# Optimization experiments

Measured on AMD Instinct MI355X. Metric: run time of the kernel, lower is better.

Reference implementation:

```python
import jax, jax.numpy as jnp
import numpy as np

D_MODEL = 1024
NUM_HEADS = 16
HEAD_DIM = D_MODEL // NUM_HEADS
B, L = 2, 2048


def setup_inputs() -> dict:
    key = jax.random.key(0)
    ks = jax.random.split(key, 9)
    s = 0.02
    return {
        "query": jax.random.normal(ks[0], (B, L, D_MODEL), dtype=jnp.float32),
        "key": jax.random.normal(ks[1], (B, L, D_MODEL), dtype=jnp.float32),
        "value": jax.random.normal(ks[2], (B, L, D_MODEL), dtype=jnp.float32),
        "mask": jax.random.randint(ks[3], (B, L), 0, 2, dtype=jnp.int32),
        "Wq": jax.random.normal(ks[4], (D_MODEL, D_MODEL), dtype=jnp.float32) * s,
        "Wk": jax.random.normal(ks[5], (D_MODEL, D_MODEL), dtype=jnp.float32) * s,
        "Wv": jax.random.normal(ks[6], (D_MODEL, D_MODEL), dtype=jnp.float32) * s,
        "Wo": jax.random.normal(ks[7], (D_MODEL, D_MODEL), dtype=jnp.float32) * s,
        "bo": jnp.zeros((D_MODEL,), dtype=jnp.float32),
    }


def _split_heads(x):
    # (B, L, d_model) -> (B, H, L, head_dim)
    b, l, _ = x.shape
    return x.reshape(b, l, NUM_HEADS, HEAD_DIM).transpose(0, 2, 1, 3)


def reference(query, key, value, mask, Wq, Wk, Wv, Wo, bo):
    # nn.Linear(bias=False): x @ W.T
    q = _split_heads(query @ Wq.T)   # (B, H, L, hd)
    k = _split_heads(key @ Wk.T)
    v = _split_heads(value @ Wv.T)

    scores = jnp.einsum("bhqd,bhkd->bhqk", q, k) / jnp.sqrt(jnp.float32(HEAD_DIM))
    # padding mask over keys: (B, L) -> (B, 1, 1, L); 0 = pad -> -inf
    keep = (mask[:, None, None, :] != 0)
    scores = jnp.where(keep, scores, -jnp.inf)

    attn = jax.nn.softmax(scores, axis=-1)
    # original zeroes NaN rows (fully-masked query rows)
    attn = jnp.where(jnp.isnan(attn), jnp.zeros_like(attn), attn)
    # dropout is identity in eval/reference mode

    ctx = jnp.einsum("bhqk,bhkd->bhqd", attn, v)           # (B, H, L, hd)
    ctx = ctx.transpose(0, 2, 1, 3).reshape(B, L, D_MODEL)  # combine heads
    return ctx @ Wo.T + bo
```

## Files before the change

kernel.cpp:

```cpp
#include <hip/hip_runtime.h>

typedef unsigned short u16;
typedef __bf16 bf16x8 __attribute__((ext_vector_type(8)));
typedef __bf16 bf16x4 __attribute__((ext_vector_type(4)));
typedef float floatx4 __attribute__((ext_vector_type(4)));
typedef u16 u16x4 __attribute__((ext_vector_type(4)));

#define MEG ((size_t)(1u << 20))

__device__ __forceinline__ u16 f2bf(float f) {
  unsigned int u = __float_as_uint(f);
  u += 0x7fffu + ((u >> 16) & 1u);
  return (u16)(u >> 16);
}

__device__ __forceinline__ void load_lds16(const u16* g, u16* l) {
  __builtin_amdgcn_global_load_lds((const __attribute__((address_space(1))) unsigned int*)g,
                                   (__attribute__((address_space(3))) unsigned int*)l,
                                   16, 0, 0);
}

__global__ __launch_bounds__(256) void cvt7(
    const float* __restrict__ s0, const float* __restrict__ s1,
    const float* __restrict__ s2, const float* __restrict__ s3,
    const float* __restrict__ s4, const float* __restrict__ s5,
    const float* __restrict__ s6, u16* __restrict__ dst)
{
  size_t e = ((size_t)blockIdx.x * 256 + threadIdx.x) * 4;
  unsigned m = (unsigned)(e >> 20);
  const float* s; size_t off;
  if (m < 4)       { s = s0; off = e; }
  else if (m < 8)  { s = s1; off = e - 4 * MEG; }
  else if (m < 12) { s = s2; off = e - 8 * MEG; }
  else if (m < 13) { s = s3; off = e - 12 * MEG; }
  else if (m < 14) { s = s4; off = e - 13 * MEG; }
  else if (m < 15) { s = s5; off = e - 14 * MEG; }
  else             { s = s6; off = e - 15 * MEG; }
  float4 f = *reinterpret_cast<const float4*>(s + off);
  u16x4 o;
  o.x = f2bf(f.x); o.y = f2bf(f.y); o.z = f2bf(f.z); o.w = f2bf(f.w);
  *reinterpret_cast<u16x4*>(dst + e) = o;
}

template<int IT, bool OUT_BF16, bool ADD_BIAS, bool VT>
__global__ __launch_bounds__(256) void gemm_bt(
    const u16* __restrict__ Abase, const u16* __restrict__ Bbase,
    const float* __restrict__ bias, void* __restrict__ Cbase,
    u16* __restrict__ VtB,
    int M, int N, int K, long zA, long zB, long zC)
{
  __shared__ __align__(16) u16 As[IT * 32 * 64];
  __shared__ __align__(16) u16 Bs[128 * 64];
  const int tid = threadIdx.x;
  const int w = tid >> 6, ln = tid & 63;
  const int lm = ln & 15, lq = ln >> 4;
  const int wm = w >> 1, wn = w & 1;
  const long m0 = (long)blockIdx.y * (IT * 32), n0 = (long)blockIdx.x * 128;
  const u16* A = Abase + (size_t)blockIdx.z * (size_t)zA;
  const u16* B = Bbase + (size_t)blockIdx.z * (size_t)zB;

  const int r0 = tid >> 3;
  const int kc = (tid & 7) ^ (r0 & 7);
  const u16* gA = A + (m0 + r0) * (long)K + kc * 8;
  const u16* gB = B + (n0 + r0) * (long)K + kc * 8;
  const long rstep = 32L * K;

  const int sl0 = (lq ^ (lm & 7)) * 8;
  const int sl1 = ((4 + lq) ^ (lm & 7)) * 8;
  const u16* ab0 = &As[(wm * (IT * 16) + lm) * 64 + sl0];
  const u16* ab1 = &As[(wm * (IT * 16) + lm) * 64 + sl1];
  const u16* bb0 = &Bs[(wn * 64 + lm) * 64 + sl0];
  const u16* bb1 = &Bs[(wn * 64 + lm) * 64 + sl1];

  const floatx4 z4 = {0.f, 0.f, 0.f, 0.f};
  floatx4 acc[IT][4];
#pragma unroll
  for (int i = 0; i < IT; ++i)
#pragma unroll
    for (int j = 0; j < 4; ++j) acc[i][j] = z4;

  for (int k0 = 0; k0 < K; k0 += 64) {
#pragma unroll
    for (int t = 0; t < IT; ++t)
      load_lds16(gA + t * rstep, &As[(t * 256 + w * 64) * 8]);
#pragma unroll
    for (int t = 0; t < 4; ++t)
      load_lds16(gB + t * rstep, &Bs[(t * 256 + w * 64) * 8]);
    gA += 64; gB += 64;
    __syncthreads();
    bf16x8 af[IT][2], bfr[4][2];
#pragma unroll
    for (int i = 0; i < IT; ++i) {
      af[i][0] = *reinterpret_cast<const bf16x8*>(ab0 + i * 1024);
      af[i][1] = *reinterpret_cast<const bf16x8*>(ab1 + i * 1024);
    }
#pragma unroll
    for (int j = 0; j < 4; ++j) {
      bfr[j][0] = *reinterpret_cast<const bf16x8*>(bb0 + j * 1024);
      bfr[j][1] = *reinterpret_cast<const bf16x8*>(bb1 + j * 1024);
    }
#pragma unroll
    for (int i = 0; i < IT; ++i)
#pragma unroll
      for (int j = 0; j < 4; ++j) {
        acc[i][j] = __builtin_amdgcn_mfma_f32_16x16x32_bf16(af[i][0], bfr[j][0], acc[i][j], 0, 0, 0);
        acc[i][j] = __builtin_amdgcn_mfma_f32_16x16x32_bf16(af[i][1], bfr[j][1], acc[i][j], 0, 0, 0);
      }
    __syncthreads();
  }

  if (VT && blockIdx.z == 2) {
#pragma unroll
    for (int i = 0; i < IT; ++i) {
      long row = m0 + wm * (IT * 16) + i * 16 + lq * 4;
      int bq = (int)(row >> 11);
      int l  = (int)(row & 2047);
#pragma unroll
      for (int j = 0; j < 4; ++j) {
        long col = n0 + wn * 64 + j * 16 + lm;
        int hh = (int)(col >> 6), dd = (int)(col & 63);
        u16x4 o;
        o.x = f2bf(acc[i][j][0]); o.y = f2bf(acc[i][j][1]);
        o.z = f2bf(acc[i][j][2]); o.w = f2bf(acc[i][j][3]);
        *reinterpret_cast<u16x4*>(&VtB[((size_t)(bq * 16 + hh)) * 131072 +
                                       (size_t)dd * 2048 + l]) = o;
      }
    }
    return;
  }

#pragma unroll
  for (int i = 0; i < IT; ++i) {
    long row = m0 + wm * (IT * 16) + i * 16 + lq * 4;
#pragma unroll
    for (int j = 0; j < 4; ++j) {
      long col = n0 + wn * 64 + j * 16 + lm;
#pragma unroll
      for (int r = 0; r < 4; ++r) {
        float v = acc[i][j][r];
        if (ADD_BIAS) v += bias[col];
        size_t idx = (size_t)(row + r) * (size_t)N + (size_t)col;
        if (OUT_BF16) (((u16*)Cbase) + (size_t)blockIdx.z * (size_t)zC)[idx] = f2bf(v);
        else ((float*)Cbase)[idx] = v;
      }
    }
  }
}

__global__ __launch_bounds__(256, 4) void attn_kernel(
    const u16* __restrict__ Qp, const u16* __restrict__ Kp,
    const u16* __restrict__ Vt, const int* __restrict__ mask,
    u16* __restrict__ ctx)
{
  __shared__ __align__(16) u16 Ks[64 * 64];
  __shared__ __align__(16) u16 Vts[64 * 64];
  __shared__ __align__(16) u16 Ps[4 * 32 * 64];
  __shared__ __align__(16) u16 mball[2048];

  const int tid = threadIdx.x;
  const int w = tid >> 6, ln = tid & 63;
  const int lm = ln & 15, lq = ln >> 4;
  const int bh = blockIdx.y, b = bh >> 4, h = bh & 15;
  const int q0 = blockIdx.x * 128;

  const u16* Qh = Qp + (size_t)b * 2048 * 1024 + h * 64;
  const u16* Kh = Kp + (size_t)b * 2048 * 1024 + h * 64;
  const u16* Vth = Vt + (size_t)bh * 64 * 2048;

  const int* mrowp = mask + b * 2048;
#pragma unroll
  for (int t = 0; t < 8; ++t) {
    int i = t * 256 + tid;
    mball[i] = (mrowp[i] != 0) ? (u16)0 : (u16)0xFF80;
  }

  bf16x8 qf[2][2];
#pragma unroll
  for (int m = 0; m < 2; ++m) {
    int qrow = q0 + w * 32 + m * 16 + lm;
    qf[m][0] = *reinterpret_cast<const bf16x8*>(Qh + (size_t)qrow * 1024 + lq * 8);
    qf[m][1] = *reinterpret_cast<const bf16x8*>(Qh + (size_t)qrow * 1024 + 32 + lq * 8);
  }

  const int sl0 = (lq ^ (lm & 7)) * 8;
  const int sl1 = ((4 + lq) ^ (lm & 7)) * 8;
  const u16* kb0 = &Ks[lm * 64 + sl0];
  const u16* kb1 = &Ks[lm * 64 + sl1];
  const u16* vb0 = &Vts[lm * 64 + sl0];
  const u16* vb1 = &Vts[lm * 64 + sl1];
  u16* Pw = &Ps[w * 2048];
  u16* pwr[4];
#pragma unroll
  for (int n = 0; n < 4; ++n) pwr[n] = &Pw[lm * 64 + (((4 * n + lq) ^ lm) * 4)];
  const u16* prd[4];
#pragma unroll
  for (int t = 0; t < 4; ++t)
    prd[t] = &Pw[lm * 64 + (((8 * (t >> 1) + 2 * lq + (t & 1)) ^ lm) * 4)];
  const u16* mbi = mball + lq * 4;

  const int r0 = tid >> 3;
  const int kc = (tid & 7) ^ (r0 & 7);
  const u16* gK0 = Kh + (size_t)r0 * 1024 + kc * 8;
  const u16* gK1 = gK0 + 32 * 1024;
  const u16* gV0 = Vth + (size_t)r0 * 2048 + kc * 8;
  const u16* gV1 = gV0 + 32 * 2048;

  const floatx4 z4 = {0.f, 0.f, 0.f, 0.f};
  floatx4 O[2][4];
#pragma unroll
  for (int m = 0; m < 2; ++m)
#pragma unroll
    for (int j = 0; j < 4; ++j) O[m][j] = z4;
  float psum[2] = {0.f, 0.f};
  const float SCL = 0.18033688011112042f;

  for (int it = 0; it < 32; ++it) {
    load_lds16(gK0, &Ks[(w * 64) * 8]);
    load_lds16(gK1, &Ks[(256 + w * 64) * 8]);
    load_lds16(gV0, &Vts[(w * 64) * 8]);
    load_lds16(gV1, &Vts[(256 + w * 64) * 8]);
    gK0 += 64 * 1024; gK1 += 64 * 1024; gV0 += 64; gV1 += 64;
    __syncthreads();

    bf16x8 kf[4][2], vf[4][2];
#pragma unroll
    for (int n = 0; n < 4; ++n) {
      kf[n][0] = *reinterpret_cast<const bf16x8*>(kb0 + n * 1024);
      kf[n][1] = *reinterpret_cast<const bf16x8*>(kb1 + n * 1024);
    }
#pragma unroll
    for (int j = 0; j < 4; ++j) {
      vf[j][0] = *reinterpret_cast<const bf16x8*>(vb0 + j * 1024);
      vf[j][1] = *reinterpret_cast<const bf16x8*>(vb1 + j * 1024);
    }
    float mb4[4][4];
#pragma unroll
    for (int n = 0; n < 4; ++n) {
      u16x4 mv = *reinterpret_cast<const u16x4*>(mbi + n * 16);
      mb4[n][0] = __uint_as_float((unsigned)mv.x << 16);
      mb4[n][1] = __uint_as_float((unsigned)mv.y << 16);
      mb4[n][2] = __uint_as_float((unsigned)mv.z << 16);
      mb4[n][3] = __uint_as_float((unsigned)mv.w << 16);
    }

#pragma unroll
    for (int m = 0; m < 2; ++m) {
      floatx4 S[4];
#pragma unroll
      for (int n = 0; n < 4; ++n) {
        S[n] = __builtin_amdgcn_mfma_f32_16x16x32_bf16(kf[n][0], qf[m][0], z4, 0, 0, 0);
        S[n] = __builtin_amdgcn_mfma_f32_16x16x32_bf16(kf[n][1], qf[m][1], S[n], 0, 0, 0);
      }

#pragma unroll
      for (int n = 0; n < 4; ++n) {
        float p0 = __builtin_amdgcn_exp2f(fmaf(S[n][0], SCL, mb4[n][0]));
        float p1 = __builtin_amdgcn_exp2f(fmaf(S[n][1], SCL, mb4[n][1]));
        float p2 = __builtin_amdgcn_exp2f(fmaf(S[n][2], SCL, mb4[n][2]));
        float p3 = __builtin_amdgcn_exp2f(fmaf(S[n][3], SCL, mb4[n][3]));
        psum[m] += (p0 + p1) + (p2 + p3);
        unsigned u0 = __float_as_uint(p0) + 0x8000u;
        unsigned u1 = __float_as_uint(p1) + 0x8000u;
        unsigned u2 = __float_as_uint(p2) + 0x8000u;
        unsigned u3 = __float_as_uint(p3) + 0x8000u;
        uint2 pk;
        pk.x = __builtin_amdgcn_perm(u1, u0, 0x07060302u);
        pk.y = __builtin_amdgcn_perm(u3, u2, 0x07060302u);
        *reinterpret_cast<uint2*>(pwr[n] + m * 1024) = pk;
      }

#pragma unroll
      for (int h2 = 0; h2 < 2; ++h2) {
        bf16x4 pa = *reinterpret_cast<const bf16x4*>(prd[2 * h2] + m * 1024);
        bf16x4 pb = *reinterpret_cast<const bf16x4*>(prd[2 * h2 + 1] + m * 1024);
        bf16x8 pf = __builtin_shufflevector(pa, pb, 0, 1, 2, 3, 4, 5, 6, 7);
#pragma unroll
        for (int j = 0; j < 4; ++j)
          O[m][j] = __builtin_amdgcn_mfma_f32_16x16x32_bf16(pf, vf[j][h2], O[m][j], 0, 0, 0);
      }
    }
    mbi += 64;
    __syncthreads();
  }

#pragma unroll
  for (int m = 0; m < 2; ++m) {
    float s = psum[m];
    s += __shfl_xor(s, 16, 64);
    s += __shfl_xor(s, 32, 64);
#pragma unroll
    for (int r = 0; r < 4; ++r) {
      int srcl = (ln & 48) | (lq * 4 + r);
      float inv = 1.0f / __shfl(s, srcl, 64);
      int row = q0 + w * 32 + m * 16 + lq * 4 + r;
      size_t base = ((size_t)b * 2048 + row) * 1024 + h * 64 + lm;
#pragma unroll
      for (int j = 0; j < 4; ++j)
        ctx[base + j * 16] = f2bf(O[m][j][r] * inv);
    }
  }
}

extern "C" void kernel_launch(void* const* d_in, const int* in_sizes, int n_in,
                              void* d_out, int out_size, void* d_ws, size_t ws_size,
                              hipStream_t stream) {
  const float* q  = (const float*)d_in[0];
  const float* k  = (const float*)d_in[1];
  const float* v  = (const float*)d_in[2];
  const int*   mk = (const int*)  d_in[3];
  const float* wq = (const float*)d_in[4];
  const float* wk = (const float*)d_in[5];
  const float* wv = (const float*)d_in[6];
  const float* wo = (const float*)d_in[7];
  const float* bo = (const float*)d_in[8];

  u16* ws16 = (u16*)d_ws;
  u16* Xq  = ws16;
  u16* Wq  = ws16 + 12 * MEG;
  u16* Wo  = ws16 + 15 * MEG;
  u16* Qp  = ws16 + 16 * MEG;
  u16* Kp  = ws16 + 20 * MEG;
  u16* Vt  = ws16 + 24 * MEG;
  u16* ctx = ws16 + 4 * MEG;

  cvt7<<<dim3(16384), dim3(256), 0, stream>>>(q, k, v, wq, wk, wv, wo, ws16);

  gemm_bt<4, true, false, true><<<dim3(8, 32, 3), dim3(256), 0, stream>>>(
      Xq, Wq, nullptr, (void*)Qp, Vt, 4096, 1024, 1024,
      (long)(4 * MEG), (long)MEG, (long)(4 * MEG));

  attn_kernel<<<dim3(16, 32), dim3(256), 0, stream>>>(Qp, Kp, Vt, mk, ctx);

  gemm_bt<2, false, true, false><<<dim3(8, 64, 1), dim3(256), 0, stream>>>(
      ctx, Wo, bo, d_out, nullptr, 4096, 1024, 1024, 0, 0, 0);
}
```

Measured before the change: 230.8 us.

## Use single-wave attention blocks loading K/V fragments directly from global memory

Shrinks the attention kernel from four-wave blocks with shared K/V tiles in LDS to one-wave blocks. Each wave now loads its K and V MFMA fragments straight from global memory, which removes the LDS staging and both block barriers per iteration. The trade-off is that every wave re-reads K/V instead of four waves sharing them, giving roughly four times the K/V global/L2 traffic. It also guards the final normalization against a zero row sum, so fully masked rows produce zero.

```diff
diff --git a/kernel.cpp b/kernel.cpp
--- a/kernel.cpp
+++ b/kernel.cpp
@@ -147,21 +147,18 @@
   }
 }
 
-__global__ __launch_bounds__(256, 4) void attn_kernel(
+__global__ __launch_bounds__(64) void attn_kernel(
     const u16* __restrict__ Qp, const u16* __restrict__ Kp,
     const u16* __restrict__ Vt, const int* __restrict__ mask,
     u16* __restrict__ ctx)
 {
-  __shared__ __align__(16) u16 Ks[64 * 64];
-  __shared__ __align__(16) u16 Vts[64 * 64];
-  __shared__ __align__(16) u16 Ps[4 * 32 * 64];
+  __shared__ __align__(16) u16 Ps[32 * 64];
   __shared__ __align__(16) u16 mball[2048];
 
-  const int tid = threadIdx.x;
-  const int w = tid >> 6, ln = tid & 63;
+  const int ln = threadIdx.x;
   const int lm = ln & 15, lq = ln >> 4;
   const int bh = blockIdx.y, b = bh >> 4, h = bh & 15;
-  const int q0 = blockIdx.x * 128;
+  const int q0 = blockIdx.x * 32;
 
   const u16* Qh = Qp + (size_t)b * 2048 * 1024 + h * 64;
   const u16* Kh = Kp + (size_t)b * 2048 * 1024 + h * 64;
@@ -169,41 +166,36 @@
 
   const int* mrowp = mask + b * 2048;
 #pragma unroll
-  for (int t = 0; t < 8; ++t) {
-    int i = t * 256 + tid;
+  for (int t = 0; t < 32; ++t) {
+    int i = t * 64 + ln;
     mball[i] = (mrowp[i] != 0) ? (u16)0 : (u16)0xFF80;
   }
 
   bf16x8 qf[2][2];
 #pragma unroll
   for (int m = 0; m < 2; ++m) {
-    int qrow = q0 + w * 32 + m * 16 + lm;
+    int qrow = q0 + m * 16 + lm;
     qf[m][0] = *reinterpret_cast<const bf16x8*>(Qh + (size_t)qrow * 1024 + lq * 8);
     qf[m][1] = *reinterpret_cast<const bf16x8*>(Qh + (size_t)qrow * 1024 + 32 + lq * 8);
   }
 
-  const int sl0 = (lq ^ (lm & 7)) * 8;
-  const int sl1 = ((4 + lq) ^ (lm & 7)) * 8;
-  const u16* kb0 = &Ks[lm * 64 + sl0];
-  const u16* kb1 = &Ks[lm * 64 + sl1];
-  const u16* vb0 = &Vts[lm * 64 + sl0];
-  const u16* vb1 = &Vts[lm * 64 + sl1];
-  u16* Pw = &Ps[w * 2048];
+  const u16* kptr[4];
+#pragma unroll
+  for (int n = 0; n < 4; ++n)
+    kptr[n] = Kh + (size_t)(n * 16 + lm) * 1024 + lq * 8;
+  const u16* vptr[4];
+#pragma unroll
+  for (int j = 0; j < 4; ++j)
+    vptr[j] = Vth + (size_t)(j * 16 + lm) * 2048 + lq * 8;
+
   u16* pwr[4];
 #pragma unroll
-  for (int n = 0; n < 4; ++n) pwr[n] = &Pw[lm * 64 + (((4 * n + lq) ^ lm) * 4)];
+  for (int n = 0; n < 4; ++n) pwr[n] = &Ps[lm * 64 + (((4 * n + lq) ^ lm) * 4)];
   const u16* prd[4];
 #pragma unroll
   for (int t = 0; t < 4; ++t)
-    prd[t] = &Pw[lm * 64 + (((8 * (t >> 1) + 2 * lq + (t & 1)) ^ lm) * 4)];
+    prd[t] = &Ps[lm * 64 + (((8 * (t >> 1) + 2 * lq + (t & 1)) ^ lm) * 4)];
   const u16* mbi = mball + lq * 4;
-
-  const int r0 = tid >> 3;
-  const int kc = (tid & 7) ^ (r0 & 7);
-  const u16* gK0 = Kh + (size_t)r0 * 1024 + kc * 8;
-  const u16* gK1 = gK0 + 32 * 1024;
-  const u16* gV0 = Vth + (size_t)r0 * 2048 + kc * 8;
-  const u16* gV1 = gV0 + 32 * 2048;
 
   const floatx4 z4 = {0.f, 0.f, 0.f, 0.f};
   floatx4 O[2][4];
@@ -215,23 +207,18 @@
   const float SCL = 0.18033688011112042f;
 
   for (int it = 0; it < 32; ++it) {
-    load_lds16(gK0, &Ks[(w * 64) * 8]);
-    load_lds16(gK1, &Ks[(256 + w * 64) * 8]);
-    load_lds16(gV0, &Vts[(w * 64) * 8]);
-    load_lds16(gV1, &Vts[(256 + w * 64) * 8]);
-    gK0 += 64 * 1024; gK1 += 64 * 1024; gV0 += 64; gV1 += 64;
-    __syncthreads();
-
     bf16x8 kf[4][2], vf[4][2];
 #pragma unroll
     for (int n = 0; n < 4; ++n) {
-      kf[n][0] = *reinterpret_cast<const bf16x8*>(kb0 + n * 1024);
-      kf[n][1] = *reinterpret_cast<const bf16x8*>(kb1 + n * 1024);
+      kf[n][0] = *reinterpret_cast<const bf16x8*>(kptr[n]);
+      kf[n][1] = *reinterpret_cast<const bf16x8*>(kptr[n] + 32);
+      kptr[n] += 64 * 1024;
     }
 #pragma unroll
     for (int j = 0; j < 4; ++j) {
-      vf[j][0] = *reinterpret_cast<const bf16x8*>(vb0 + j * 1024);
-      vf[j][1] = *reinterpret_cast<const bf16x8*>(vb1 + j * 1024);
+      vf[j][0] = *reinterpret_cast<const bf16x8*>(vptr[j]);
+      vf[j][1] = *reinterpret_cast<const bf16x8*>(vptr[j] + 32);
+      vptr[j] += 64;
     }
     float mb4[4][4];
 #pragma unroll
@@ -242,6 +229,7 @@
       mb4[n][2] = __uint_as_float((unsigned)mv.z << 16);
       mb4[n][3] = __uint_as_float((unsigned)mv.w << 16);
     }
+    mbi += 64;
 
 #pragma unroll
     for (int m = 0; m < 2; ++m) {
@@ -279,8 +267,6 @@
           O[m][j] = __builtin_amdgcn_mfma_f32_16x16x32_bf16(pf, vf[j][h2], O[m][j], 0, 0, 0);
       }
     }
-    mbi += 64;
-    __syncthreads();
   }
 
 #pragma unroll
@@ -291,8 +277,9 @@
 #pragma unroll
     for (int r = 0; r < 4; ++r) {
       int srcl = (ln & 48) | (lq * 4 + r);
-      float inv = 1.0f / __shfl(s, srcl, 64);
-      int row = q0 + w * 32 + m * 16 + lq * 4 + r;
+      float sv = __shfl(s, srcl, 64);
+      float inv = (sv > 0.f) ? 1.0f / sv : 0.f;
+      int row = q0 + m * 16 + lq * 4 + r;
       size_t base = ((size_t)b * 2048 + row) * 1024 + h * 64 + lm;
 #pragma unroll
       for (int j = 0; j < 4; ++j)
@@ -329,7 +316,7 @@
       Xq, Wq, nullptr, (void*)Qp, Vt, 4096, 1024, 1024,
       (long)(4 * MEG), (long)MEG, (long)(4 * MEG));
 
-  attn_kernel<<<dim3(16, 32), dim3(256), 0, stream>>>(Qp, Kp, Vt, mk, ctx);
+  attn_kernel<<<dim3(64, 32), dim3(64), 0, stream>>>(Qp, Kp, Vt, mk, ctx);
 
   gemm_bt<2, false, true, false><<<dim3(8, 64, 1), dim3(256), 0, stream>>>(
       ctx, Wo, bo, d_out, nullptr, 4096, 1024, 1024, 0, 0, 0);
```

Result: slower. 299.3 us (+29.7%).

## Split attention key range across two blocks and combine partials in a separate kernel

Applied to the files above, without the earlier changes.

The attention kernel now splits the 2048 keys into two halves along a new grid z dimension. This doubles the block count so more CUs are occupied. Each half writes its unnormalized bf16 output and its row sums to workspace, and a new combine_norm kernel adds the two halves and normalizes, returning zero for fully masked rows. In exchange it adds one extra launch, roughly 16 MB of extra global write and read traffic, and rounds the partial outputs to bf16 before they are summed.

```diff
diff --git a/kernel.cpp b/kernel.cpp
--- a/kernel.cpp
+++ b/kernel.cpp
@@ -150,26 +150,29 @@
 __global__ __launch_bounds__(256, 4) void attn_kernel(
     const u16* __restrict__ Qp, const u16* __restrict__ Kp,
     const u16* __restrict__ Vt, const int* __restrict__ mask,
-    u16* __restrict__ ctx)
+    u16* __restrict__ OpBase, float* __restrict__ psAB)
 {
   __shared__ __align__(16) u16 Ks[64 * 64];
   __shared__ __align__(16) u16 Vts[64 * 64];
   __shared__ __align__(16) u16 Ps[4 * 32 * 64];
-  __shared__ __align__(16) u16 mball[2048];
+  __shared__ __align__(16) u16 mball[1024];
 
   const int tid = threadIdx.x;
   const int w = tid >> 6, ln = tid & 63;
   const int lm = ln & 15, lq = ln >> 4;
   const int bh = blockIdx.y, b = bh >> 4, h = bh & 15;
   const int q0 = blockIdx.x * 128;
+  const int kz = blockIdx.z;
 
   const u16* Qh = Qp + (size_t)b * 2048 * 1024 + h * 64;
-  const u16* Kh = Kp + (size_t)b * 2048 * 1024 + h * 64;
-  const u16* Vth = Vt + (size_t)bh * 64 * 2048;
-
-  const int* mrowp = mask + b * 2048;
-#pragma unroll
-  for (int t = 0; t < 8; ++t) {
+  const u16* Kh = Kp + (size_t)b * 2048 * 1024 + (size_t)kz * 1024 * 1024 + h * 64;
+  const u16* Vth = Vt + (size_t)bh * 64 * 2048 + kz * 1024;
+  u16* Op = OpBase + (size_t)kz * 8 * MEG;
+  float* psZ = psAB + (size_t)kz * 65536;
+
+  const int* mrowp = mask + b * 2048 + kz * 1024;
+#pragma unroll
+  for (int t = 0; t < 4; ++t) {
     int i = t * 256 + tid;
     mball[i] = (mrowp[i] != 0) ? (u16)0 : (u16)0xFF80;
   }
@@ -214,7 +217,7 @@
   float psum[2] = {0.f, 0.f};
   const float SCL = 0.18033688011112042f;
 
-  for (int it = 0; it < 32; ++it) {
+  for (int it = 0; it < 16; ++it) {
     load_lds16(gK0, &Ks[(w * 64) * 8]);
     load_lds16(gK1, &Ks[(256 + w * 64) * 8]);
     load_lds16(gV0, &Vts[(w * 64) * 8]);
@@ -242,6 +245,7 @@
       mb4[n][2] = __uint_as_float((unsigned)mv.z << 16);
       mb4[n][3] = __uint_as_float((unsigned)mv.w << 16);
     }
+    mbi += 64;
 
 #pragma unroll
     for (int m = 0; m < 2; ++m) {
@@ -279,7 +283,6 @@
           O[m][j] = __builtin_amdgcn_mfma_f32_16x16x32_bf16(pf, vf[j][h2], O[m][j], 0, 0, 0);
       }
     }
-    mbi += 64;
     __syncthreads();
   }
 
@@ -288,17 +291,49 @@
     float s = psum[m];
     s += __shfl_xor(s, 16, 64);
     s += __shfl_xor(s, 32, 64);
+    int prow = q0 + w * 32 + m * 16 + lm;
+    if (lq == 0) psZ[bh * 2048 + prow] = s;
 #pragma unroll
     for (int r = 0; r < 4; ++r) {
-      int srcl = (ln & 48) | (lq * 4 + r);
-      float inv = 1.0f / __shfl(s, srcl, 64);
       int row = q0 + w * 32 + m * 16 + lq * 4 + r;
       size_t base = ((size_t)b * 2048 + row) * 1024 + h * 64 + lm;
 #pragma unroll
       for (int j = 0; j < 4; ++j)
-        ctx[base + j * 16] = f2bf(O[m][j][r] * inv);
-    }
-  }
+        Op[base + j * 16] = f2bf(O[m][j][r]);
+    }
+  }
+}
+
+__global__ __launch_bounds__(256) void combine_norm(
+    const u16* __restrict__ Oa, const u16* __restrict__ Ob,
+    const float* __restrict__ psA, const float* __restrict__ psB,
+    u16* __restrict__ ctx)
+{
+  size_t idx = ((size_t)blockIdx.x * 256 + threadIdx.x) * 8;
+  int q = (int)(idx >> 10);
+  int c = (int)(idx & 1023);
+  int b = q >> 11, l = q & 2047, h = c >> 6;
+  int ql = (b * 16 + h) * 2048 + l;
+  float s = psA[ql] + psB[ql];
+  float inv = (s > 0.f) ? 1.0f / s : 0.f;
+
+  uint4 ua = *reinterpret_cast<const uint4*>(Oa + idx);
+  uint4 ub = *reinterpret_cast<const uint4*>(Ob + idx);
+  uint4 uo;
+  const unsigned* pa = reinterpret_cast<const unsigned*>(&ua);
+  const unsigned* pb = reinterpret_cast<const unsigned*>(&ub);
+  unsigned* po = reinterpret_cast<unsigned*>(&uo);
+#pragma unroll
+  for (int i = 0; i < 4; ++i) {
+    float alo = __uint_as_float(pa[i] << 16);
+    float ahi = __uint_as_float(pa[i] & 0xFFFF0000u);
+    float blo = __uint_as_float(pb[i] << 16);
+    float bhi = __uint_as_float(pb[i] & 0xFFFF0000u);
+    float olo = (alo + blo) * inv;
+    float ohi = (ahi + bhi) * inv;
+    po[i] = (unsigned)f2bf(olo) | ((unsigned)f2bf(ohi) << 16);
+  }
+  *reinterpret_cast<uint4*>(ctx + idx) = uo;
 }
 
 extern "C" void kernel_launch(void* const* d_in, const int* in_sizes, int n_in,
@@ -321,6 +356,9 @@
   u16* Qp  = ws16 + 16 * MEG;
   u16* Kp  = ws16 + 20 * MEG;
   u16* Vt  = ws16 + 24 * MEG;
+  u16* OpA = ws16;
+  u16* OpB = ws16 + 8 * MEG;
+  float* psAB = (float*)(ws16 + 12 * MEG);
   u16* ctx = ws16 + 4 * MEG;
 
   cvt7<<<dim3(16384), dim3(256), 0, stream>>>(q, k, v, wq, wk, wv, wo, ws16);
@@ -329,7 +367,9 @@
       Xq, Wq, nullptr, (void*)Qp, Vt, 4096, 1024, 1024,
       (long)(4 * MEG), (long)MEG, (long)(4 * MEG));
 
-  attn_kernel<<<dim3(16, 32), dim3(256), 0, stream>>>(Qp, Kp, Vt, mk, ctx);
+  attn_kernel<<<dim3(16, 32, 2), dim3(256), 0, stream>>>(Qp, Kp, Vt, mk, OpA, psAB);
+
+  combine_norm<<<dim3(2048), dim3(256), 0, stream>>>(OpA, OpB, psAB, psAB + 65536, ctx);
 
   gemm_bt<2, false, true, false><<<dim3(8, 64, 1), dim3(256), 0, stream>>>(
       ctx, Wo, bo, d_out, nullptr, 4096, 1024, 1024, 0, 0, 0);
```

New measurement: 222.6 us. 1.04x faster.
